# Kernel tuning notes

Hardware: AMD Instinct MI355X
Metric: run time of the kernel (lower is better)

Reference implementation:

```python
import math
import jax, jax.numpy as jnp
import numpy as np

K = 3
ROTATIONS = np.array([i * math.pi / 4.0 for i in range(8)], dtype=np.float32)
SCALES = np.array([1.0, 1.25, 1.25**2, 1.25**3], dtype=np.float32)


def setup_inputs() -> dict:
    key = jax.random.key(0)
    k1, k2 = jax.random.split(key)
    x = jax.random.normal(k1, (8, 32, 512, 512), dtype=jnp.float32)
    freq_weight = jax.random.normal(k2, (32, 32, K, K // 2 + 1, 2), dtype=jnp.float32) * 0.02
    return {"x": x, "freq_weight": freq_weight}


def _spatial_kernel(freq_weight):
    # view_as_complex over last dim, then 2D inverse rFFT to a k x k spatial kernel
    cw = freq_weight[..., 0] + 1j * freq_weight[..., 1]
    return jnp.fft.irfft2(cw, s=(K, K), axes=(-2, -1))  # (O, I, K, K), real


def _transform_kernel(kernel, cos_t, sin_t):
    # F.affine_grid + F.grid_sample (bilinear, zeros padding, align_corners=False)
    k = K
    # output pixel centers in normalized coords, align_corners=False
    coords = (2.0 * jnp.arange(k, dtype=kernel.dtype) + 1.0) / k - 1.0  # (k,)
    gy_out, gx_out = jnp.meshgrid(coords, coords, indexing="ij")  # (k, k)
    # affine theta = [[c, -s, 0], [s, c, 0]] applied to (x, y, 1)
    gx = cos_t * gx_out - sin_t * gy_out
    gy = sin_t * gx_out + cos_t * gy_out
    # unnormalize (align_corners=False)
    ix = ((gx + 1.0) * k - 1.0) * 0.5
    iy = ((gy + 1.0) * k - 1.0) * 0.5
    x0 = jnp.floor(ix).astype(jnp.int32)
    y0 = jnp.floor(iy).astype(jnp.int32)
    x1, y1 = x0 + 1, y0 + 1
    wx1 = ix - x0.astype(kernel.dtype)
    wy1 = iy - y0.astype(kernel.dtype)
    wx0, wy0 = 1.0 - wx1, 1.0 - wy1

    def tap(yy, xx):
        valid = (xx >= 0) & (xx < k) & (yy >= 0) & (yy < k)
        v = kernel[..., jnp.clip(yy, 0, k - 1), jnp.clip(xx, 0, k - 1)]  # (O, I, k, k)
        return jnp.where(valid, v, jnp.zeros((), kernel.dtype))

    return (tap(y0, x0) * (wy0 * wx0)
            + tap(y0, x1) * (wy0 * wx1)
            + tap(y1, x0) * (wy1 * wx0)
            + tap(y1, x1) * (wy1 * wx1))


def _equivariant_kernel(freq_weight):
    base = _spatial_kernel(freq_weight)
    th = jnp.asarray(ROTATIONS)[:, None]  # (8, 1)
    sc = jnp.asarray(SCALES)[None, :]     # (1, 4)
    cos_t = (jnp.cos(th) * sc).reshape(-1)  # (32,)
    sin_t = (jnp.sin(th) * sc).reshape(-1)
    kernels = jax.vmap(lambda c, s: _transform_kernel(base, c, s))(cos_t, sin_t)
    return kernels.mean(axis=0)  # (O, I, K, K)


def reference(x, freq_weight):
    kern = _equivariant_kernel(freq_weight)
    pad = K // 2
    return jax.lax.conv_general_dilated(
        x, kern, window_strides=(1, 1), padding=[(pad, pad), (pad, pad)],
        dimension_numbers=("NCHW", "OIHW", "NCHW"))
```

## Files before the change

kernel.cpp:

```cpp
#include <hip/hip_runtime.h>
#include <hip/hip_bf16.h>


typedef __attribute__((ext_vector_type(8))) short bf16x8;
typedef __attribute__((ext_vector_type(16))) float f32x16;
typedef __attribute__((ext_vector_type(4))) unsigned int u32x4;
typedef __attribute__((ext_vector_type(4))) float f32x4v;

__device__ __forceinline__ unsigned short f2bf(float f) {
    unsigned u = __float_as_uint(f);
    u = u + 0x7fffu + ((u >> 16) & 1u);
    return (unsigned short)(u >> 16);
}
__device__ __forceinline__ float bf2f(unsigned short b) {
    return __uint_as_float(((unsigned)b) << 16);
}

__device__ __forceinline__ void lgkm_barrier() {
    asm volatile("s_waitcnt lgkmcnt(0)" ::: "memory");
    __builtin_amdgcn_s_barrier();
    __builtin_amdgcn_sched_barrier(0);
}

__global__ __launch_bounds__(256) void prep_kernel(const float* __restrict__ fw,
                                                   unsigned short* __restrict__ wbuf)
{
    int gid = blockIdx.x * blockDim.x + threadIdx.x;
    if (gid >= 32 * 32) return;
    int o = gid >> 5;
    int i = gid & 31;

    const float* f = fw + (size_t)gid * 12;
    float re[3][2], im[3][2];
#pragma unroll
    for (int ky = 0; ky < 3; ++ky)
#pragma unroll
        for (int kx = 0; kx < 2; ++kx) {
            re[ky][kx] = f[(ky * 2 + kx) * 2 + 0];
            im[ky][kx] = f[(ky * 2 + kx) * 2 + 1];
        }

    const float c3[3] = {1.f, -0.5f, -0.5f};
    const float s3[3] = {0.f, 0.86602540378443864676f, -0.86602540378443864676f};

    float base[3][3];
#pragma unroll
    for (int y = 0; y < 3; ++y)
#pragma unroll
        for (int x = 0; x < 3; ++x) {
            float sum = 0.f;
#pragma unroll
            for (int ky = 0; ky < 3; ++ky)
#pragma unroll
                for (int kx = 0; kx < 3; ++kx) {
                    float rf, mf;
                    if (kx < 2) {
                        rf = re[ky][kx];
                        mf = im[ky][kx];
                    } else {
                        int kys = (3 - ky) % 3;
                        rf = re[kys][1];
                        mf = -im[kys][1];
                    }
                    int m = (ky * y + kx * x) % 3;
                    sum += rf * c3[m] - mf * s3[m];
                }
            base[y][x] = sum * (1.f / 9.f);
        }

    const float scales[4] = {1.f, 1.25f, 1.5625f, 1.953125f};
    const float coords[3] = {-2.f / 3.f, 0.f, 2.f / 3.f};

    float acc[3][3] = {{0.f, 0.f, 0.f}, {0.f, 0.f, 0.f}, {0.f, 0.f, 0.f}};

    for (int t = 0; t < 32; ++t) {
        int r = t >> 2, si = t & 3;
        float th = (float)r * 0.78539816339744830961f;
        float sc = scales[si];
        float c = cosf(th) * sc;
        float s = sinf(th) * sc;
#pragma unroll
        for (int p = 0; p < 3; ++p) {
#pragma unroll
            for (int q = 0; q < 3; ++q) {
                float gxo = coords[q], gyo = coords[p];
                float gx = c * gxo - s * gyo;
                float gy = s * gxo + c * gyo;
                float ix = ((gx + 1.f) * 3.f - 1.f) * 0.5f;
                float iy = ((gy + 1.f) * 3.f - 1.f) * 0.5f;
                float fx0 = floorf(ix), fy0 = floorf(iy);
                int x0 = (int)fx0, y0 = (int)fy0;
                int x1 = x0 + 1, y1 = y0 + 1;
                float wx1 = ix - fx0, wy1 = iy - fy0;
                float wx0 = 1.f - wx1, wy0 = 1.f - wy1;

                float v = 0.f;
                {
                    int yc = min(max(y0, 0), 2), xc = min(max(x0, 0), 2);
                    bool ok = (x0 >= 0) & (x0 < 3) & (y0 >= 0) & (y0 < 3);
                    v += (ok ? base[yc][xc] : 0.f) * (wy0 * wx0);
                }
                {
                    int yc = min(max(y0, 0), 2), xc = min(max(x1, 0), 2);
                    bool ok = (x1 >= 0) & (x1 < 3) & (y0 >= 0) & (y0 < 3);
                    v += (ok ? base[yc][xc] : 0.f) * (wy0 * wx1);
                }
                {
                    int yc = min(max(y1, 0), 2), xc = min(max(x0, 0), 2);
                    bool ok = (x0 >= 0) & (x0 < 3) & (y1 >= 0) & (y1 < 3);
                    v += (ok ? base[yc][xc] : 0.f) * (wy1 * wx0);
                }
                {
                    int yc = min(max(y1, 0), 2), xc = min(max(x1, 0), 2);
                    bool ok = (x1 >= 0) & (x1 < 3) & (y1 >= 0) & (y1 < 3);
                    v += (ok ? base[yc][xc] : 0.f) * (wy1 * wx1);
                }
                acc[p][q] += v;
            }
        }
    }

#pragma unroll
    for (int p = 0; p < 3; ++p)
#pragma unroll
        for (int q = 0; q < 3; ++q) {
            int t = p * 3 + q;
            float w = acc[p][q] * (1.f / 32.f);
            unsigned short wh = f2bf(w);
            unsigned short wl = f2bf(w - bf2f(wh));
            size_t b = (size_t)(t * 2) * 1024 + o * 32 + i;
            wbuf[b] = wh;
            wbuf[b + 1024] = wl;
        }
}

#define ROWB 2176
#define BUFB 21760

__device__ __forceinline__ unsigned swz(int px, int c) {
    return ((unsigned)px << 6) + ((((unsigned)(px >> 1) & 3u) ^ (unsigned)c) << 4);
}

__global__ __launch_bounds__(256, 2) void conv_pipe(const float* __restrict__ x,
                                                    const unsigned short* __restrict__ wbuf,
                                                    float* __restrict__ out)
{
    __shared__ char lds[2 * BUFB];

    const int lin = blockIdx.x;
    const int n = lin & 7;
    const int idx = lin >> 3;
    const int xt = idx & 15;
    const int yseg = idx >> 4;
    const int x0t = xt * 32;
    const int Y0 = yseg * 64;

    const int tid = threadIdx.x;
    const int lane = tid & 63;
    const int wv = tid >> 6;
    const int pxl = lane & 31;
    const int kh = lane >> 5;

    const float* xn = x + ((size_t)n << 23);

    bf16x8 A[3][3][2];
#pragma unroll
    for (int dy = 0; dy < 3; ++dy)
#pragma unroll
        for (int dx = 0; dx < 3; ++dx)
#pragma unroll
            for (int ks = 0; ks < 2; ++ks)
                A[dy][dx][ks] = *(const bf16x8*)(
                    wbuf + (size_t)((dy * 3 + dx) * 2) * 1024 +
                    pxl * 32 + ks * 16 + kh * 8);

    int coff[3];
#pragma unroll
    for (int dx = 0; dx < 3; ++dx) {
        int v = dx + pxl - 1;
        int pl = (v < 0) ? 32 : ((v == 32) ? 33 : v);
        coff[dx] = (int)swz(pl, kh);
    }

    for (int u = tid; u < 400; u += 256) {
        if (u < 320) {
            int row = u >> 5, q = (u >> 2) & 7, c = u & 3;
            int gy = Y0 - 1 + row;
            bool ok = (unsigned)gy < 512u;
            const float* src = xn + (((size_t)(c * 8)) << 18) + ((ok ? gy : 0) << 9) +
                               x0t + (q << 2);
            float v[8][4];
#pragma unroll
            for (int cc = 0; cc < 8; ++cc) {
                f32x4v ld = *(const f32x4v*)(src + ((size_t)cc << 18));
#pragma unroll
                for (int j = 0; j < 4; ++j) v[cc][j] = ok ? ld[j] : 0.f;
            }
            int px0 = (q << 2);
#pragma unroll
            for (int j = 0; j < 4; ++j) {
                u32x4 d;
#pragma unroll
                for (int p = 0; p < 4; ++p)
                    d[p] = (unsigned)f2bf(v[2 * p][j]) | ((unsigned)f2bf(v[2 * p + 1][j]) << 16);
                *(u32x4*)(lds + row * ROWB + swz(px0 + j, c)) = d;
            }
        } else {
            int hu = u - 320;
            int row = hu >> 3, side = (hu >> 2) & 1, c = hu & 3;
            int gy = Y0 - 1 + row;
            int gx = x0t + (side ? 32 : -1);
            bool ok = ((unsigned)gy < 512u) & ((unsigned)gx < 512u);
            const float* src = xn + (((size_t)(c * 8)) << 18) +
                               ((ok ? gy : 0) << 9) + (ok ? gx : 0);
            u32x4 d;
#pragma unroll
            for (int p = 0; p < 4; ++p) {
                float a = ok ? src[(size_t)(2 * p) << 18] : 0.f;
                float b = ok ? src[(size_t)(2 * p + 1) << 18] : 0.f;
                d[p] = (unsigned)f2bf(a) | ((unsigned)f2bf(b) << 16);
            }
            *(u32x4*)(lds + row * ROWB + swz(32 + side, c)) = d;
        }
    }
    lgkm_barrier();

#pragma unroll 1
    for (int t = 0; t < 8; ++t) {
        const int R = Y0 + (t << 3);
        const bool st = (t < 7);
        const char* rbuf = lds + (t & 1) * BUFB;
        char* wlds = lds + ((t + 1) & 1) * BUFB;

        f32x4v L0[8], L1[8];
        float H[8];
        int r0s = 0, q0 = 0, c0 = 0, r1s = 0, q1 = 0, c1 = 0;
        int hr = 0, hside = 0, hc = 0;
        bool ok0 = false, ok1 = false, okh = false;
        const int kind = (tid < 64) ? 1 : (tid < 144 ? 2 : 0);
        if (st) {
            r0s = tid >> 5; q0 = (tid >> 2) & 7; c0 = tid & 3;
            int gy = R + 7 + r0s;
            ok0 = (unsigned)gy < 512u;
            const float* src = xn + (((size_t)(c0 * 8)) << 18) + ((ok0 ? gy : 0) << 9) +
                               x0t + (q0 << 2);
#pragma unroll
            for (int cc = 0; cc < 8; ++cc) L0[cc] = *(const f32x4v*)(src + ((size_t)cc << 18));
            if (kind == 1) {
                int u = 256 + tid;
                r1s = u >> 5; q1 = (u >> 2) & 7; c1 = u & 3;
                int gy1 = R + 7 + r1s;
                ok1 = (unsigned)gy1 < 512u;
                const float* s1 = xn + (((size_t)(c1 * 8)) << 18) + ((ok1 ? gy1 : 0) << 9) +
                                  x0t + (q1 << 2);
#pragma unroll
                for (int cc = 0; cc < 8; ++cc) L1[cc] = *(const f32x4v*)(s1 + ((size_t)cc << 18));
            } else if (kind == 2) {
                int hu = tid - 64;
                hr = hu >> 3; hside = (hu >> 2) & 1; hc = hu & 3;
                int gy1 = R + 7 + hr;
                int gx = x0t + (hside ? 32 : -1);
                okh = ((unsigned)gy1 < 512u) & ((unsigned)gx < 512u);
                const float* s1 = xn + (((size_t)(hc * 8)) << 18) +
                                  ((okh ? gy1 : 0) << 9) + (okh ? gx : 0);
#pragma unroll
                for (int cc = 0; cc < 8; ++cc) H[cc] = s1[(size_t)cc << 18];
            }
        }
        __builtin_amdgcn_sched_barrier(0);

        f32x16 acc[2];
#pragma unroll
        for (int f = 0; f < 2; ++f)
#pragma unroll
            for (int r = 0; r < 16; ++r) acc[f][r] = 0.f;

#pragma unroll
        for (int m = 0; m < 4; ++m) {
            const int rs = (wv << 1) + m;
            bf16x8 b[3][2];
#pragma unroll
            for (int dx = 0; dx < 3; ++dx)
#pragma unroll
                for (int ks = 0; ks < 2; ++ks)
                    b[dx][ks] = *(const bf16x8*)(rbuf + rs * ROWB +
                                                 (unsigned)(coff[dx] ^ (ks << 5)));
#pragma unroll
            for (int f = 0; f < 2; ++f) {
                const int dy = m - f;
                if (dy >= 0 && dy < 3) {
#pragma unroll
                    for (int dx = 0; dx < 3; ++dx)
#pragma unroll
                        for (int ks = 0; ks < 2; ++ks)
                            acc[f] = __builtin_amdgcn_mfma_f32_32x32x16_bf16(
                                A[dy][dx][ks], b[dx][ks], acc[f], 0, 0, 0);
                }
            }
        }

        if (st) {
            {
                int px0 = (q0 << 2);
#pragma unroll
                for (int j = 0; j < 4; ++j) {
                    u32x4 d;
#pragma unroll
                    for (int p = 0; p < 4; ++p) {
                        float a = ok0 ? L0[2 * p][j] : 0.f;
                        float b2 = ok0 ? L0[2 * p + 1][j] : 0.f;
                        d[p] = (unsigned)f2bf(a) | ((unsigned)f2bf(b2) << 16);
                    }
                    *(u32x4*)(wlds + r0s * ROWB + swz(px0 + j, c0)) = d;
                }
            }
            if (kind == 1) {
                int px0 = (q1 << 2);
#pragma unroll
                for (int j = 0; j < 4; ++j) {
                    u32x4 d;
#pragma unroll
                    for (int p = 0; p < 4; ++p) {
                        float a = ok1 ? L1[2 * p][j] : 0.f;
                        float b2 = ok1 ? L1[2 * p + 1][j] : 0.f;
                        d[p] = (unsigned)f2bf(a) | ((unsigned)f2bf(b2) << 16);
                    }
                    *(u32x4*)(wlds + r1s * ROWB + swz(px0 + j, c1)) = d;
                }
            } else if (kind == 2) {
                u32x4 d;
#pragma unroll
                for (int p = 0; p < 4; ++p) {
                    float a = okh ? H[2 * p] : 0.f;
                    float b2 = okh ? H[2 * p + 1] : 0.f;
                    d[p] = (unsigned)f2bf(a) | ((unsigned)f2bf(b2) << 16);
                }
                *(u32x4*)(wlds + hr * ROWB + swz(32 + hside, hc)) = d;
            }
        }

#pragma unroll
        for (int f = 0; f < 2; ++f) {
            int gy = R + (wv << 1) + f;
#pragma unroll
            for (int reg = 0; reg < 16; ++reg) {
                int o = (reg & 3) + 8 * (reg >> 2) + 4 * kh;
                size_t oidx = ((size_t)(n * 32 + o) << 18) + ((size_t)gy << 9) + x0t + pxl;
                __builtin_nontemporal_store(acc[f][reg], &out[oidx]);
            }
        }

        lgkm_barrier();
    }
}

extern "C" void kernel_launch(void* const* d_in, const int* in_sizes, int n_in,
                              void* d_out, int out_size, void* d_ws, size_t ws_size,
                              hipStream_t stream) {
    const float* x = (const float*)d_in[0];
    const float* fw = (const float*)d_in[1];
    float* out = (float*)d_out;
    unsigned short* wbuf = (unsigned short*)d_ws;

    prep_kernel<<<dim3(4), 256, 0, stream>>>(fw, wbuf);
    conv_pipe<<<dim3(1024), 256, 0, stream>>>(x, wbuf, out);
}
```

Baseline: 189.9 us.

## Prefetch next stripe's global loads one iteration earlier in the row loop

Global loads of input rows for the next stripe are moved into the prologue and issued at the end of each iteration, after the LDS writes, instead of at the top of the iteration. This gives them a whole iteration (including output stores and barrier) to land in registers, deepening the software pipeline. The load registers stay live across the MFMA section, which may raise register pressure and lower occupancy.

```diff
diff --git a/kernel.cpp b/kernel.cpp
--- a/kernel.cpp
+++ b/kernel.cpp
@@ -182,6 +182,13 @@
         coff[dx] = (int)swz(pl, kh);
     }
 
+    const int r0s = tid >> 5, q0 = (tid >> 2) & 7, c0 = tid & 3;
+    const int kind = (tid < 64) ? 1 : (tid < 144 ? 2 : 0);
+    const int u1 = 256 + tid;
+    const int r1s = u1 >> 5, q1 = (u1 >> 2) & 7, c1 = u1 & 3;
+    const int hu = tid - 64;
+    const int hr = hu >> 3, hside = (hu >> 2) & 1, hc = hu & 3;
+
     for (int u = tid; u < 400; u += 256) {
         if (u < 320) {
             int row = u >> 5, q = (u >> 2) & 7, c = u & 3;
@@ -206,8 +213,8 @@
                 *(u32x4*)(lds + row * ROWB + swz(px0 + j, c)) = d;
             }
         } else {
-            int hu = u - 320;
-            int row = hu >> 3, side = (hu >> 2) & 1, c = hu & 3;
+            int hu2 = u - 320;
+            int row = hu2 >> 3, side = (hu2 >> 2) & 1, c = hu2 & 3;
             int gy = Y0 - 1 + row;
             int gx = x0t + (side ? 32 : -1);
             bool ok = ((unsigned)gy < 512u) & ((unsigned)gx < 512u);
@@ -223,51 +230,45 @@
             *(u32x4*)(lds + row * ROWB + swz(32 + side, c)) = d;
         }
     }
+
+    f32x4v L0[8], L1[8];
+    float H[8];
+    bool ok0 = false, ok1 = false, okh = false;
+
+    {
+        const int R = Y0;
+        int gy = R + 7 + r0s;
+        ok0 = (unsigned)gy < 512u;
+        const float* src = xn + (((size_t)(c0 * 8)) << 18) + ((ok0 ? gy : 0) << 9) +
+                           x0t + (q0 << 2);
+#pragma unroll
+        for (int cc = 0; cc < 8; ++cc) L0[cc] = *(const f32x4v*)(src + ((size_t)cc << 18));
+        if (kind == 1) {
+            int gy1 = R + 7 + r1s;
+            ok1 = (unsigned)gy1 < 512u;
+            const float* s1 = xn + (((size_t)(c1 * 8)) << 18) + ((ok1 ? gy1 : 0) << 9) +
+                              x0t + (q1 << 2);
+#pragma unroll
+            for (int cc = 0; cc < 8; ++cc) L1[cc] = *(const f32x4v*)(s1 + ((size_t)cc << 18));
+        } else if (kind == 2) {
+            int gy1 = R + 7 + hr;
+            int gx = x0t + (hside ? 32 : -1);
+            okh = ((unsigned)gy1 < 512u) & ((unsigned)gx < 512u);
+            const float* s1 = xn + (((size_t)(hc * 8)) << 18) +
+                              ((okh ? gy1 : 0) << 9) + (okh ? gx : 0);
+#pragma unroll
+            for (int cc = 0; cc < 8; ++cc) H[cc] = s1[(size_t)cc << 18];
+        }
+    }
     lgkm_barrier();
 
 #pragma unroll 1
     for (int t = 0; t < 8; ++t) {
         const int R = Y0 + (t << 3);
         const bool st = (t < 7);
+        const bool st2 = (t < 6);
         const char* rbuf = lds + (t & 1) * BUFB;
         char* wlds = lds + ((t + 1) & 1) * BUFB;
-
-        f32x4v L0[8], L1[8];
-        float H[8];
-        int r0s = 0, q0 = 0, c0 = 0, r1s = 0, q1 = 0, c1 = 0;
-        int hr = 0, hside = 0, hc = 0;
-        bool ok0 = false, ok1 = false, okh = false;
-        const int kind = (tid < 64) ? 1 : (tid < 144 ? 2 : 0);
-        if (st) {
-            r0s = tid >> 5; q0 = (tid >> 2) & 7; c0 = tid & 3;
-            int gy = R + 7 + r0s;
-            ok0 = (unsigned)gy < 512u;
-            const float* src = xn + (((size_t)(c0 * 8)) << 18) + ((ok0 ? gy : 0) << 9) +
-                               x0t + (q0 << 2);
-#pragma unroll
-            for (int cc = 0; cc < 8; ++cc) L0[cc] = *(const f32x4v*)(src + ((size_t)cc << 18));
-            if (kind == 1) {
-                int u = 256 + tid;
-                r1s = u >> 5; q1 = (u >> 2) & 7; c1 = u & 3;
-                int gy1 = R + 7 + r1s;
-                ok1 = (unsigned)gy1 < 512u;
-                const float* s1 = xn + (((size_t)(c1 * 8)) << 18) + ((ok1 ? gy1 : 0) << 9) +
-                                  x0t + (q1 << 2);
-#pragma unroll
-                for (int cc = 0; cc < 8; ++cc) L1[cc] = *(const f32x4v*)(s1 + ((size_t)cc << 18));
-            } else if (kind == 2) {
-                int hu = tid - 64;
-                hr = hu >> 3; hside = (hu >> 2) & 1; hc = hu & 3;
-                int gy1 = R + 7 + hr;
-                int gx = x0t + (hside ? 32 : -1);
-                okh = ((unsigned)gy1 < 512u) & ((unsigned)gx < 512u);
-                const float* s1 = xn + (((size_t)(hc * 8)) << 18) +
-                                  ((okh ? gy1 : 0) << 9) + (okh ? gx : 0);
-#pragma unroll
-                for (int cc = 0; cc < 8; ++cc) H[cc] = s1[(size_t)cc << 18];
-            }
-        }
-        __builtin_amdgcn_sched_barrier(0);
 
         f32x16 acc[2];
 #pragma unroll
@@ -338,6 +339,33 @@
                 *(u32x4*)(wlds + hr * ROWB + swz(32 + hside, hc)) = d;
             }
         }
+
+        if (st2) {
+            const int Rn = R + 8;
+            int gy = Rn + 7 + r0s;
+            ok0 = (unsigned)gy < 512u;
+            const float* src = xn + (((size_t)(c0 * 8)) << 18) + ((ok0 ? gy : 0) << 9) +
+                               x0t + (q0 << 2);
+#pragma unroll
+            for (int cc = 0; cc < 8; ++cc) L0[cc] = *(const f32x4v*)(src + ((size_t)cc << 18));
+            if (kind == 1) {
+                int gy1 = Rn + 7 + r1s;
+                ok1 = (unsigned)gy1 < 512u;
+                const float* s1 = xn + (((size_t)(c1 * 8)) << 18) + ((ok1 ? gy1 : 0) << 9) +
+                                  x0t + (q1 << 2);
+#pragma unroll
+                for (int cc = 0; cc < 8; ++cc) L1[cc] = *(const f32x4v*)(s1 + ((size_t)cc << 18));
+            } else if (kind == 2) {
+                int gy1 = Rn + 7 + hr;
+                int gx = x0t + (hside ? 32 : -1);
+                okh = ((unsigned)gy1 < 512u) & ((unsigned)gx < 512u);
+                const float* s1 = xn + (((size_t)(hc * 8)) << 18) +
+                                  ((okh ? gy1 : 0) << 9) + (okh ? gx : 0);
+#pragma unroll
+                for (int cc = 0; cc < 8; ++cc) H[cc] = s1[(size_t)cc << 18];
+            }
+        }
+        __builtin_amdgcn_sched_barrier(0);
 
 #pragma unroll
         for (int f = 0; f < 2; ++f) {
```

Result: slower. 214.7 us (+13.1%).

## Replace double-buffered halo tiles with an 18-row LDS ring buffer

Applied to the files above, without the earlier changes.

The conv pipeline kept two full 10-row LDS buffers and reloaded all 10 input rows (8 new rows plus a 2-row halo) from global memory each 8-row step. It now keeps an 18-row circular buffer in LDS, so each step loads only the 8 new rows and the 2 halo rows are reused from the previous step. This cuts global loads, bf16 conversion work and per-thread register staging (the second load set L1 is gone). LDS use drops slightly from 43520 to 39168 bytes, at the cost of modular slot arithmetic. The prep kernel also replaces its cosf/sinf calls with constant tables of the eight rotation angles.

```diff
diff --git a/kernel.cpp b/kernel.cpp
--- a/kernel.cpp
+++ b/kernel.cpp
@@ -68,6 +68,9 @@
             base[y][x] = sum * (1.f / 9.f);
         }
 
+    const float S2 = 0.70710678118654752440f;
+    const float ctab[8] = {1.f, S2, 0.f, -S2, -1.f, -S2, 0.f, S2};
+    const float stab[8] = {0.f, S2, 1.f, S2, 0.f, -S2, -1.f, -S2};
     const float scales[4] = {1.f, 1.25f, 1.5625f, 1.953125f};
     const float coords[3] = {-2.f / 3.f, 0.f, 2.f / 3.f};
 
@@ -75,10 +78,9 @@
 
     for (int t = 0; t < 32; ++t) {
         int r = t >> 2, si = t & 3;
-        float th = (float)r * 0.78539816339744830961f;
         float sc = scales[si];
-        float c = cosf(th) * sc;
-        float s = sinf(th) * sc;
+        float c = ctab[r] * sc;
+        float s = stab[r] * sc;
 #pragma unroll
         for (int p = 0; p < 3; ++p) {
 #pragma unroll
@@ -135,7 +137,7 @@
 }
 
 #define ROWB 2176
-#define BUFB 21760
+#define RING 18
 
 __device__ __forceinline__ unsigned swz(int px, int c) {
     return ((unsigned)px << 6) + ((((unsigned)(px >> 1) & 3u) ^ (unsigned)c) << 4);
@@ -145,7 +147,7 @@
                                                     const unsigned short* __restrict__ wbuf,
                                                     float* __restrict__ out)
 {
-    __shared__ char lds[2 * BUFB];
+    __shared__ char lds[RING * ROWB];
 
     const int lin = blockIdx.x;
     const int n = lin & 7;
@@ -182,6 +184,16 @@
         coff[dx] = (int)swz(pl, kh);
     }
 
+    const int r0s = tid >> 5, q0 = (tid >> 2) & 7, c0 = tid & 3;
+    const int hr = tid >> 3, hside = (tid >> 2) & 1, hc = tid & 3;
+    const bool hk = (tid < 64);
+
+    int sl[4];
+#pragma unroll
+    for (int m = 0; m < 4; ++m) sl[m] = (Y0 + (wv << 1) + m) % 18;
+    int wb = (Y0 + 10) % 18;
+
+    const int p0 = Y0 % 18;
     for (int u = tid; u < 400; u += 256) {
         if (u < 320) {
             int row = u >> 5, q = (u >> 2) & 7, c = u & 3;
@@ -196,6 +208,7 @@
 #pragma unroll
                 for (int j = 0; j < 4; ++j) v[cc][j] = ok ? ld[j] : 0.f;
             }
+            int slot = p0 + row; if (slot >= 18) slot -= 18;
             int px0 = (q << 2);
 #pragma unroll
             for (int j = 0; j < 4; ++j) {
@@ -203,11 +216,11 @@
 #pragma unroll
                 for (int p = 0; p < 4; ++p)
                     d[p] = (unsigned)f2bf(v[2 * p][j]) | ((unsigned)f2bf(v[2 * p + 1][j]) << 16);
-                *(u32x4*)(lds + row * ROWB + swz(px0 + j, c)) = d;
+                *(u32x4*)(lds + slot * ROWB + swz(px0 + j, c)) = d;
             }
         } else {
-            int hu = u - 320;
-            int row = hu >> 3, side = (hu >> 2) & 1, c = hu & 3;
+            int hu2 = u - 320;
+            int row = hu2 >> 3, side = (hu2 >> 2) & 1, c = hu2 & 3;
             int gy = Y0 - 1 + row;
             int gx = x0t + (side ? 32 : -1);
             bool ok = ((unsigned)gy < 512u) & ((unsigned)gx < 512u);
@@ -220,7 +233,8 @@
                 float b = ok ? src[(size_t)(2 * p + 1) << 18] : 0.f;
                 d[p] = (unsigned)f2bf(a) | ((unsigned)f2bf(b) << 16);
             }
-            *(u32x4*)(lds + row * ROWB + swz(32 + side, c)) = d;
+            int slot = p0 + row; if (slot >= 18) slot -= 18;
+            *(u32x4*)(lds + slot * ROWB + swz(32 + side, c)) = d;
         }
     }
     lgkm_barrier();
@@ -229,36 +243,19 @@
     for (int t = 0; t < 8; ++t) {
         const int R = Y0 + (t << 3);
         const bool st = (t < 7);
-        const char* rbuf = lds + (t & 1) * BUFB;
-        char* wlds = lds + ((t + 1) & 1) * BUFB;
-
-        f32x4v L0[8], L1[8];
+
+        f32x4v L0[8];
         float H[8];
-        int r0s = 0, q0 = 0, c0 = 0, r1s = 0, q1 = 0, c1 = 0;
-        int hr = 0, hside = 0, hc = 0;
-        bool ok0 = false, ok1 = false, okh = false;
-        const int kind = (tid < 64) ? 1 : (tid < 144 ? 2 : 0);
+        bool ok0 = false, okh = false;
         if (st) {
-            r0s = tid >> 5; q0 = (tid >> 2) & 7; c0 = tid & 3;
-            int gy = R + 7 + r0s;
+            int gy = R + 9 + r0s;
             ok0 = (unsigned)gy < 512u;
             const float* src = xn + (((size_t)(c0 * 8)) << 18) + ((ok0 ? gy : 0) << 9) +
                                x0t + (q0 << 2);
 #pragma unroll
             for (int cc = 0; cc < 8; ++cc) L0[cc] = *(const f32x4v*)(src + ((size_t)cc << 18));
-            if (kind == 1) {
-                int u = 256 + tid;
-                r1s = u >> 5; q1 = (u >> 2) & 7; c1 = u & 3;
-                int gy1 = R + 7 + r1s;
-                ok1 = (unsigned)gy1 < 512u;
-                const float* s1 = xn + (((size_t)(c1 * 8)) << 18) + ((ok1 ? gy1 : 0) << 9) +
-                                  x0t + (q1 << 2);
-#pragma unroll
-                for (int cc = 0; cc < 8; ++cc) L1[cc] = *(const f32x4v*)(s1 + ((size_t)cc << 18));
-            } else if (kind == 2) {
-                int hu = tid - 64;
-                hr = hu >> 3; hside = (hu >> 2) & 1; hc = hu & 3;
-                int gy1 = R + 7 + hr;
+            if (hk) {
+                int gy1 = R + 9 + hr;
                 int gx = x0t + (hside ? 32 : -1);
                 okh = ((unsigned)gy1 < 512u) & ((unsigned)gx < 512u);
                 const float* s1 = xn + (((size_t)(hc * 8)) << 18) +
@@ -277,13 +274,12 @@
 
 #pragma unroll
         for (int m = 0; m < 4; ++m) {
-            const int rs = (wv << 1) + m;
             bf16x8 b[3][2];
 #pragma unroll
             for (int dx = 0; dx < 3; ++dx)
 #pragma unroll
                 for (int ks = 0; ks < 2; ++ks)
-                    b[dx][ks] = *(const bf16x8*)(rbuf + rs * ROWB +
+                    b[dx][ks] = *(const bf16x8*)(lds + sl[m] * ROWB +
                                                  (unsigned)(coff[dx] ^ (ks << 5)));
 #pragma unroll
             for (int f = 0; f < 2; ++f) {
@@ -301,6 +297,7 @@
 
         if (st) {
             {
+                int slot = wb + r0s; if (slot >= 18) slot -= 18;
                 int px0 = (q0 << 2);
 #pragma unroll
                 for (int j = 0; j < 4; ++j) {
@@ -311,23 +308,11 @@
                         float b2 = ok0 ? L0[2 * p + 1][j] : 0.f;
                         d[p] = (unsigned)f2bf(a) | ((unsigned)f2bf(b2) << 16);
                     }
-                    *(u32x4*)(wlds + r0s * ROWB + swz(px0 + j, c0)) = d;
-                }
-            }
-            if (kind == 1) {
-                int px0 = (q1 << 2);
-#pragma unroll
-                for (int j = 0; j < 4; ++j) {
-                    u32x4 d;
-#pragma unroll
-                    for (int p = 0; p < 4; ++p) {
-                        float a = ok1 ? L1[2 * p][j] : 0.f;
-                        float b2 = ok1 ? L1[2 * p + 1][j] : 0.f;
-                        d[p] = (unsigned)f2bf(a) | ((unsigned)f2bf(b2) << 16);
-                    }
-                    *(u32x4*)(wlds + r1s * ROWB + swz(px0 + j, c1)) = d;
-                }
-            } else if (kind == 2) {
+                    *(u32x4*)(lds + slot * ROWB + swz(px0 + j, c0)) = d;
+                }
+            }
+            if (hk) {
+                int slot = wb + hr; if (slot >= 18) slot -= 18;
                 u32x4 d;
 #pragma unroll
                 for (int p = 0; p < 4; ++p) {
@@ -335,7 +320,7 @@
                     float b2 = okh ? H[2 * p + 1] : 0.f;
                     d[p] = (unsigned)f2bf(a) | ((unsigned)f2bf(b2) << 16);
                 }
-                *(u32x4*)(wlds + hr * ROWB + swz(32 + hside, hc)) = d;
+                *(u32x4*)(lds + slot * ROWB + swz(32 + hside, hc)) = d;
             }
         }
 
@@ -351,6 +336,12 @@
         }
 
         lgkm_barrier();
+
+#pragma unroll
+        for (int m = 0; m < 4; ++m) {
+            sl[m] += 8; if (sl[m] >= 18) sl[m] -= 18;
+        }
+        wb += 8; if (wb >= 18) wb -= 18;
     }
 }
 
```

After: 153.5 us (median of 4 runs). 1.24x faster.
